# Performance work log

Hardware: AMD Instinct MI355X
Metric: run time of the kernel (lower is better)

Reference implementation:

```python
import jax, jax.numpy as jnp
import numpy as np

B, N, E = 2, 50000, 800000
IN_CH, SP_CH, OUT_CH, EDGE_CH = 64, 16, 32, 1


def _xavier(k, shape):
    scale = (2.0 / (shape[0] + shape[1])) ** 0.5
    return jax.random.normal(k, shape, dtype=jnp.float32) * scale


def setup_inputs() -> dict:
    key = jax.random.key(0)
    ks = jax.random.split(key, 20)
    return {
        "X": jax.random.normal(ks[0], (B, N, IN_CH), dtype=jnp.float32),
        "edge_index0": jax.random.randint(ks[1], (2, E), 0, N),
        "edge_index1": jax.random.randint(ks[2], (2, E), 0, N),
        "edge_weight0": jax.random.uniform(ks[3], (E, EDGE_CH), dtype=jnp.float32),
        "edge_weight1": jax.random.uniform(ks[4], (E, EDGE_CH), dtype=jnp.float32),
        "res_n_id0": jnp.arange(N),
        "res_n_id1": jnp.arange(N),
        # conv1 params (in=IN_CH, out=SP_CH)
        "value1": _xavier(ks[5], (IN_CH, SP_CH)),
        "key1": _xavier(ks[6], (SP_CH, SP_CH)),
        "query1": _xavier(ks[7], (SP_CH, SP_CH)),
        "we1": _xavier(ks[8], (EDGE_CH, SP_CH)),
        "att_w1": _xavier(ks[9], (3 * SP_CH, 1)),
        "att_b1": jnp.zeros((1,), jnp.float32),
        "cat_w1": _xavier(ks[10], (2 * SP_CH, SP_CH)),
        "cat_b1": jnp.zeros((SP_CH,), jnp.float32),
        # conv2 params (in=SP_CH, out=OUT_CH)
        "value2": _xavier(ks[11], (SP_CH, OUT_CH)),
        "key2": _xavier(ks[12], (OUT_CH, OUT_CH)),
        "query2": _xavier(ks[13], (OUT_CH, OUT_CH)),
        "we2": _xavier(ks[14], (EDGE_CH, OUT_CH)),
        "att_w2": _xavier(ks[15], (3 * OUT_CH, 1)),
        "att_b2": jnp.zeros((1,), jnp.float32),
        "cat_w2": _xavier(ks[16], (2 * OUT_CH, OUT_CH)),
        "cat_b2": jnp.zeros((OUT_CH,), jnp.float32),
    }


def _egnn_conv(Xs, Xd, ei, ef, value, key_w, query_w, we, att_w, att_b, cat_w, cat_b):
    # Xs: [B,Ns,Cin] source nodes, Xd: [B,Nd,Cin] dest nodes, ei: [2,E], ef: [E,edge_ch]
    xs = Xs @ value                       # [B,Ns,C]
    xd = Xd @ value                       # [B,Nd,C]
    e = ef @ we                           # [E,C]
    xj = xs[:, ei[0]]                     # [B,E,C] source gather
    xi = xd[:, ei[1]]                     # [B,E,C] dest gather
    q = xj @ query_w                      # note: original code names are swapped; kept faithful
    k = xi @ key_w
    att_in = jnp.concatenate([k, q, jnp.broadcast_to(e, q.shape)], axis=-1)  # [B,E,3C]
    att = jax.nn.sigmoid(att_in @ att_w + att_b)      # [B,E,1]
    msg = att * xj * jax.nn.sigmoid(e)                # [B,E,C]
    aggr = jnp.zeros(xd.shape, xd.dtype).at[:, ei[1]].add(msg)  # scatter-add over dest
    upd = jnp.concatenate([xd, aggr], axis=-1) @ cat_w + cat_b  # [B,Nd,C]
    return xd + jax.nn.relu(upd)


def reference(X, edge_index0, edge_index1, edge_weight0, edge_weight1,
              res_n_id0, res_n_id1,
              value1, key1, query1, we1, att_w1, att_b1, cat_w1, cat_b1,
              value2, key2, query2, we2, att_w2, att_b2, cat_w2, cat_b2):
    X1 = _egnn_conv(X, X[:, res_n_id0], edge_index0, edge_weight0,
                    value1, key1, query1, we1, att_w1, att_b1, cat_w1, cat_b1)
    X1 = jax.nn.leaky_relu(X1)  # negative_slope 0.01, matches torch default
    X2 = _egnn_conv(X1, X1[:, res_n_id1], edge_index1, edge_weight1,
                    value2, key2, query2, we2, att_w2, att_b2, cat_w2, cat_b2)
    return X2
```

## Files before the change

kernel.cpp:

```cpp
#include <hip/hip_runtime.h>
#include <hip/hip_fp16.h>

#define BB   2
#define NN   50000
#define EE   800000
#define INCH 64
#define C1   16
#define C2   32
#define NB   (BB*NN)

#define W1S   6
#define W2S   5
#define NBK1  ((NN + 63) >> 6)
#define NBK2  ((NN + 31) >> 5)
#define NBKT  (NBK1 + NBK2)
#define EB    4096
#define TPB   1024
#define NEBLK ((2*EE + EB - 1) / EB)

#define OFF_XS1   0
#define OFF_XS2   (OFF_XS1 + NB*C1/2)
#define OFF_DOTK1 (OFF_XS2 + NB*C2/2)
#define OFF_DOTQ1 (OFF_DOTK1 + NB)
#define OFF_DOTK2 (OFF_DOTQ1 + NB)
#define OFF_DOTQ2 (OFF_DOTK2 + NB)
#define OFF_AG1   (OFF_DOTQ2 + NB)
#define OFF_AG2   (OFF_AG1 + NN*32)
#define OFF_BTOT  (OFF_AG2 + NN*64)
#define OFF_BBASE (OFF_BTOT + NBKT)
#define OFF_START (OFF_BBASE + NBKT)
#define OFF_DEG   (OFF_START + 2*NN)
#define OFF_SC    (OFF_DEG + 2*NN)
#define OFF_RECS2 (OFF_SC + 2)
#define OFF_REGION (OFF_RECS2 + 2*EE*2)
#define OFF_RECS   OFF_REGION
#define OFF_BCNT   (OFF_REGION + 2*EE*2)
#define OFF_PREC   OFF_REGION

__device__ __forceinline__ float sigmoidf(float x) {
    return __builtin_amdgcn_rcpf(1.0f + __expf(-x));
}

__device__ __forceinline__ float h2f_u(unsigned u) {
    return __half2float(__ushort_as_half((unsigned short)u));
}

__global__ __launch_bounds__(TPB) void k_value1cnt(
        const float* __restrict__ X, const float* __restrict__ value1,
        const float* __restrict__ key1, const float* __restrict__ query1,
        const float* __restrict__ aw1,
        const int* __restrict__ ei0, const int* __restrict__ ei1,
        const float* __restrict__ we1, const float* __restrict__ we2,
        const float* __restrict__ aw2,
        __half* __restrict__ xs1h, float* __restrict__ dotk1,
        float* __restrict__ dotq1, unsigned* __restrict__ blockCnt,
        float* __restrict__ sc) {
    __shared__ float W[INCH*C1];
    __shared__ float KV[C1], QV[C1];
    __shared__ unsigned h[NBKT];
    int tid = threadIdx.x;
    if (tid < 256) {
        for (int i = tid; i < INCH*C1; i += 256) W[i] = value1[i];
        if (tid < C1) {
            float kv = 0.f, qv = 0.f;
#pragma unroll
            for (int j = 0; j < C1; ++j) {
                kv += key1[tid*C1+j]   * aw1[j];
                qv += query1[tid*C1+j] * aw1[C1+j];
            }
            KV[tid] = kv; QV[tid] = qv;
        }
    } else {
        for (int i = tid - 256; i < NBKT; i += 768) h[i] = 0u;
        if (blockIdx.x == 0 && tid == 256) {
            float e = 0.f;
            for (int j = 0; j < C1; ++j) e += we1[j] * aw1[2*C1+j];
            sc[0] = e;
        }
        if (blockIdx.x == 0 && tid == 257) {
            float e = 0.f;
            for (int j = 0; j < C2; ++j) e += we2[j] * aw2[2*C2+j];
            sc[1] = e;
        }
    }
    __syncthreads();
    if (tid < 256) {
        int bn = blockIdx.x * 256 + tid;
        if (bn < NB) {
            int b = (bn >= NN) ? 1 : 0;
            int node = bn - b*NN;
            const float4* Xr = (const float4*)(X + (size_t)bn * INCH);
            float acc[C1];
#pragma unroll
            for (int j = 0; j < C1; ++j) acc[j] = 0.f;
#pragma unroll
            for (int v = 0; v < 16; ++v) {
                float4 p = Xr[v];
                float x4[4] = {p.x, p.y, p.z, p.w};
#pragma unroll
                for (int hh = 0; hh < 4; ++hh) {
                    int i = v*4 + hh;
                    float xv = x4[hh];
#pragma unroll
                    for (int j = 0; j < C1; ++j) acc[j] += xv * W[i*C1+j];
                }
            }
            float dk = 0.f, dq = 0.f;
#pragma unroll
            for (int j = 0; j < C1; ++j) { dk += acc[j]*KV[j]; dq += acc[j]*QV[j]; }
            __half* o = xs1h + ((size_t)node * C1) * 2 + b;
#pragma unroll
            for (int j = 0; j < C1; ++j) o[2*j] = __float2half_rn(acc[j]);
            dotk1[node*2 + b] = dk; dotq1[node*2 + b] = dq;
        }
    } else {
        int base = blockIdx.x * EB;
        for (int j = tid - 256; j < EB; j += 768) {
            int t = base + j;
            if (t < 2*EE) {
                int bkt;
                if (t < EE) { int dst = ei0[EE + t];      bkt = dst >> W1S; }
                else        { int dst = ei1[EE + t - EE]; bkt = NBK1 + (dst >> W2S); }
                atomicAdd(&h[bkt], 1u);
            }
        }
    }
    __syncthreads();
    unsigned* o = blockCnt + (size_t)blockIdx.x * NBKT;
    for (int i = tid; i < NBKT; i += TPB) o[i] = h[i];
}

__global__ __launch_bounds__(512) void k_scanBkt(
        unsigned* __restrict__ blockCnt, unsigned* __restrict__ bktTot) {
    __shared__ unsigned s[512];
    int tid = threadIdx.x;
    int bkt = blockIdx.x;
    unsigned v = (tid < NEBLK) ? blockCnt[(size_t)tid * NBKT + bkt] : 0u;
    s[tid] = v;
    __syncthreads();
    for (int o = 1; o < 512; o <<= 1) {
        unsigned t = (tid >= o) ? s[tid - o] : 0u;
        __syncthreads();
        s[tid] += t;
        __syncthreads();
    }
    if (tid < NEBLK) blockCnt[(size_t)tid * NBKT + bkt] = s[tid] - v;
    if (tid == 511) bktTot[bkt] = s[511];
}

__global__ __launch_bounds__(1024) void k_scanTot(
        const unsigned* __restrict__ bktTot, unsigned* __restrict__ bucketBase) {
    __shared__ unsigned s[1024];
    int tid = threadIdx.x;
    int base = tid * 3;
    unsigned a0 = (base + 0 < NBKT) ? bktTot[base + 0] : 0u;
    unsigned a1 = (base + 1 < NBKT) ? bktTot[base + 1] : 0u;
    unsigned a2 = (base + 2 < NBKT) ? bktTot[base + 2] : 0u;
    unsigned l = a0 + a1 + a2;
    s[tid] = l;
    __syncthreads();
    for (int o = 1; o < 1024; o <<= 1) {
        unsigned t = (tid >= o) ? s[tid - o] : 0u;
        __syncthreads();
        s[tid] += t;
        __syncthreads();
    }
    unsigned ex = s[tid] - l;
    if (base + 0 < NBKT) bucketBase[base + 0] = ex;
    if (base + 1 < NBKT) bucketBase[base + 1] = ex + a0;
    if (base + 2 < NBKT) bucketBase[base + 2] = ex + a0 + a1;
}

__global__ __launch_bounds__(TPB) void k_permute(
        const int* __restrict__ ei0, const int* __restrict__ ei1,
        const float* __restrict__ ew0, const float* __restrict__ ew1,
        const unsigned* __restrict__ blockOff, const unsigned* __restrict__ bucketBase,
        uint2* __restrict__ recs) {
    __shared__ unsigned off[NBKT];
    __shared__ unsigned cur[NBKT];
    int tid = threadIdx.x;
    const unsigned* bo = blockOff + (size_t)blockIdx.x * NBKT;
    for (int i = tid; i < NBKT; i += TPB) { off[i] = bo[i] + bucketBase[i]; cur[i] = 0u; }
    __syncthreads();
    int base = blockIdx.x * EB;
#pragma unroll
    for (int j = 0; j < EB/TPB; ++j) {
        int t = base + j*TPB + tid;
        if (t >= 2*EE) break;
        int bkt, dl, src; float ef;
        if (t < EE) {
            int dst = ei0[EE + t];
            bkt = dst >> W1S; dl = dst & 63;
            src = ei0[t]; ef = ew0[t];
        } else {
            int e = t - EE;
            int dst = ei1[EE + e];
            bkt = NBK1 + (dst >> W2S); dl = dst & 31;
            src = ei1[e]; ef = ew1[e];
        }
        unsigned pos = off[bkt] + atomicAdd(&cur[bkt], 1u);
        recs[pos] = make_uint2((unsigned)src | ((unsigned)dl << 16), __float_as_uint(ef));
    }
}

__global__ __launch_bounds__(256) void k_sortbp(
        const uint2* __restrict__ recs, const unsigned* __restrict__ bktTot,
        const unsigned* __restrict__ bucketBase,
        const float* __restrict__ dotk1, const float* __restrict__ dotq1,
        const float* __restrict__ ab1, const float* __restrict__ sc,
        uint2* __restrict__ recs2, unsigned* __restrict__ startA,
        unsigned* __restrict__ degA) {
    __shared__ unsigned h[64], sOff[64], cur[64];
    int tid = threadIdx.x;
    int bkt = blockIdx.x;
    int lay1 = (bkt < NBK1) ? 1 : 0;
    int ndl  = lay1 ? 64 : 32;
    int nodeBase = lay1 ? (bkt << W1S) : ((bkt - NBK1) << W2S);
    int layOff   = lay1 ? 0 : NN;
    if (tid < 64) h[tid] = 0u;
    __syncthreads();
    unsigned cnt = bktTot[bkt], base = bucketBase[bkt];
    for (unsigned i = tid; i < cnt; i += 256)
        atomicAdd(&h[recs[base + i].x >> 16], 1u);
    __syncthreads();
    if (tid == 0) {
        unsigned run = 0;
        for (int d = 0; d < ndl; ++d) { sOff[d] = run; run += h[d]; }
    }
    __syncthreads();
    if (tid < ndl) {
        cur[tid] = sOff[tid];
        int node = nodeBase + tid;
        if (node < NN) {
            startA[layOff + node] = base + sOff[tid];
            degA[layOff + node]   = h[tid];
        }
    }
    __syncthreads();
    float ec = sc[0], ab0 = ab1[0];
    for (unsigned i = tid; i < cnt; i += 256) {
        uint2 r = recs[base + i];
        unsigned dl  = r.x >> 16;
        unsigned src = r.x & 0xffffu;
        unsigned pos = atomicAdd(&cur[dl], 1u);
        unsigned dst = (unsigned)nodeBase + dl;
        if (lay1) {
            float ef = __uint_as_float(r.y);
            float eb = ef * ec + ab0;
            float2 dk = *(const float2*)(dotk1 + dst*2);
            float2 dq = *(const float2*)(dotq1 + src*2);
            float p0 = sigmoidf(dk.x + dq.x + eb);
            float p1 = sigmoidf(dk.y + dq.y + eb);
            unsigned pu = __builtin_bit_cast(unsigned, __floats2half2_rn(p0, p1));
            unsigned eu = (unsigned)__half_as_ushort(__float2half_rn(ef));
            recs2[base + pos] = make_uint2(src | (pu << 16),
                                           (pu >> 16) | (eu << 16));
        } else {
            recs2[base + pos] = make_uint2(src | (dst << 16), r.y);
        }
    }
}

__global__ __launch_bounds__(256) void k_prep(
        const uint2* __restrict__ recs2seg, const float* __restrict__ dotk,
        const float* __restrict__ dotq, const float* __restrict__ ab,
        const float* __restrict__ sc, int scIdx, uint2* __restrict__ prec) {
    int e = blockIdx.x * 256 + threadIdx.x;
    uint2 r = recs2seg[e];
    int src = r.x & 0xffff, dst = r.x >> 16;
    float ef = __uint_as_float(r.y);
    float eb = ef * sc[scIdx] + ab[0];
    float2 dk = *(const float2*)(dotk + dst*2);
    float2 dq = *(const float2*)(dotq + src*2);
    float p0 = sigmoidf(dk.x + dq.x + eb);
    float p1 = sigmoidf(dk.y + dq.y + eb);
    unsigned pu = __builtin_bit_cast(unsigned, __floats2half2_rn(p0, p1));
    unsigned eu = (unsigned)__half_as_ushort(__float2half_rn(ef));
    prec[e] = make_uint2((unsigned)src | (pu << 16),
                         (pu >> 16) | (eu << 16));
}

__global__ __launch_bounds__(256) void k_aggr1f(
        const uint2* __restrict__ prec, const float* __restrict__ we,
        const uint2* __restrict__ xsh,
        const unsigned* __restrict__ startA, const unsigned* __restrict__ degA,
        float* __restrict__ aggrf) {
    int t = blockIdx.x * 256 + threadIdx.x;
    int node = t >> 4, sub = t & 15, cp = sub & 7, h = sub >> 3;
    unsigned s = startA[node];
    unsigned n = degA[node];
    float w0 = we[2*cp], w1 = we[2*cp+1];
    float a0 = 0.f, a1 = 0.f, a2 = 0.f, a3 = 0.f;
    unsigned i = (unsigned)h;
    uint2 r_n = make_uint2(0u, 0u); uint2 xr_n = make_uint2(0u, 0u);
    if (i < n) {
        r_n  = prec[s + i];
        xr_n = xsh[(size_t)(r_n.x & 0xffff)*8 + cp];
    }
    for (; i < n; i += 2) {
        uint2 r = r_n; uint2 xr = xr_n;
        if (i + 2 < n) {
            r_n  = prec[s + i + 2];
            xr_n = xsh[(size_t)(r_n.x & 0xffff)*8 + cp];
        }
        float p0 = h2f_u(r.x >> 16);
        float p1 = h2f_u(r.y & 0xffff);
        float ef = h2f_u(r.y >> 16);
        float se0 = sigmoidf(ef * w0);
        float se1 = sigmoidf(ef * w1);
        float2 f0 = __half22float2(__builtin_bit_cast(__half2, xr.x));
        float2 f1 = __half22float2(__builtin_bit_cast(__half2, xr.y));
        a0 += p0 * se0 * f0.x;
        a1 += p1 * se0 * f0.y;
        a2 += p0 * se1 * f1.x;
        a3 += p1 * se1 * f1.y;
    }
    a0 += __shfl_xor(a0, 8); a1 += __shfl_xor(a1, 8);
    a2 += __shfl_xor(a2, 8); a3 += __shfl_xor(a3, 8);
    if (h == 0)
        ((float4*)aggrf)[(size_t)node*8 + cp] = make_float4(a0, a1, a2, a3);
}

__global__ __launch_bounds__(256) void k_update1(
        const float* __restrict__ cat_w, const float* __restrict__ cat_b,
        const float* __restrict__ value2,
        const float* __restrict__ key2, const float* __restrict__ query2,
        const float* __restrict__ aw2,
        const __half* __restrict__ xs1h, const float* __restrict__ aggr1f,
        __half* __restrict__ xs2h, float* __restrict__ dotk2, float* __restrict__ dotq2) {
    __shared__ float CW[2*C1*C1];
    __shared__ float CB[C1];
    __shared__ float V2[C1*C2];
    __shared__ float KV[C2], QV[C2];
    int tid = threadIdx.x;
    for (int i = tid; i < 2*C1*C1; i += 256) CW[i] = cat_w[i];
    for (int i = tid; i < C1*C2;   i += 256) V2[i] = value2[i];
    if (tid < C1) CB[tid] = cat_b[tid];
    if (tid < C2) {
        float kv = 0.f;
#pragma unroll
        for (int j = 0; j < C2; ++j) kv += key2[tid*C2+j] * aw2[j];
        KV[tid] = kv;
    } else if (tid < 2*C2) {
        int c = tid - C2;
        float qv = 0.f;
#pragma unroll
        for (int j = 0; j < C2; ++j) qv += query2[c*C2+j] * aw2[C2+j];
        QV[c] = qv;
    }
    __syncthreads();
    int bn = blockIdx.x * 256 + tid;
    if (bn >= NB) return;
    int b = (bn >= NN) ? 1 : 0;
    int node = bn - b*NN;
    int bs = b * 16;
    float xd[C1], ag[C1];
    {
        const uint4* xv = (const uint4*)(xs1h + (size_t)node * C1 * 2);
#pragma unroll
        for (int v = 0; v < 4; ++v) {
            uint4 q = xv[v];
            xd[4*v+0] = h2f_u(q.x >> bs);
            xd[4*v+1] = h2f_u(q.y >> bs);
            xd[4*v+2] = h2f_u(q.z >> bs);
            xd[4*v+3] = h2f_u(q.w >> bs);
        }
    }
    {
        const float4* av = (const float4*)(aggr1f + (size_t)node * 32);
#pragma unroll
        for (int w = 0; w < 8; ++w) {
            float4 f = av[w];
            ag[2*w]   = b ? f.y : f.x;
            ag[2*w+1] = b ? f.w : f.z;
        }
    }
    float x1[C1];
#pragma unroll
    for (int j = 0; j < C1; ++j) {
        float u = CB[j];
#pragma unroll
        for (int i = 0; i < C1; ++i) {
            u += xd[i] * CW[i*C1 + j];
            u += ag[i] * CW[(C1+i)*C1 + j];
        }
        float o = xd[j] + fmaxf(u, 0.f);
        x1[j] = (o > 0.f) ? o : 0.01f * o;
    }
    float o2[C2];
#pragma unroll
    for (int k = 0; k < C2; ++k) o2[k] = 0.f;
#pragma unroll
    for (int j = 0; j < C1; ++j) {
        float xv = x1[j];
#pragma unroll
        for (int k = 0; k < C2; ++k) o2[k] += xv * V2[j*C2 + k];
    }
    float dk = 0.f, dq = 0.f;
#pragma unroll
    for (int k = 0; k < C2; ++k) { dk += o2[k]*KV[k]; dq += o2[k]*QV[k]; }
    __half* o = xs2h + ((size_t)node*C2)*2 + b;
#pragma unroll
    for (int k = 0; k < C2; ++k) o[2*k] = __float2half_rn(o2[k]);
    dotk2[node*2 + b] = dk; dotq2[node*2 + b] = dq;
}

__global__ __launch_bounds__(256) void k_aggr2f(
        const uint2* __restrict__ prec, const float* __restrict__ we,
        const uint2* __restrict__ xsh,
        const unsigned* __restrict__ startA, const unsigned* __restrict__ degA,
        float* __restrict__ aggrf) {
    int t = blockIdx.x * 256 + threadIdx.x;
    int node = t >> 5, sub = t & 31, cp = sub & 15, h = sub >> 4;
    unsigned s = startA[NN + node] - EE;
    unsigned n = degA[NN + node];
    float w0 = we[2*cp], w1 = we[2*cp+1];
    float a0 = 0.f, a1 = 0.f, a2 = 0.f, a3 = 0.f;
    unsigned i = (unsigned)h;
    uint2 r_n = make_uint2(0u, 0u); uint2 xr_n = make_uint2(0u, 0u);
    if (i < n) {
        r_n  = prec[s + i];
        xr_n = xsh[(size_t)(r_n.x & 0xffff)*16 + cp];
    }
    for (; i < n; i += 2) {
        uint2 r = r_n; uint2 xr = xr_n;
        if (i + 2 < n) {
            r_n  = prec[s + i + 2];
            xr_n = xsh[(size_t)(r_n.x & 0xffff)*16 + cp];
        }
        float p0 = h2f_u(r.x >> 16);
        float p1 = h2f_u(r.y & 0xffff);
        float ef = h2f_u(r.y >> 16);
        float se0 = sigmoidf(ef * w0);
        float se1 = sigmoidf(ef * w1);
        float2 f0 = __half22float2(__builtin_bit_cast(__half2, xr.x));
        float2 f1 = __half22float2(__builtin_bit_cast(__half2, xr.y));
        a0 += p0 * se0 * f0.x;
        a1 += p1 * se0 * f0.y;
        a2 += p0 * se1 * f1.x;
        a3 += p1 * se1 * f1.y;
    }
    a0 += __shfl_xor(a0, 16); a1 += __shfl_xor(a1, 16);
    a2 += __shfl_xor(a2, 16); a3 += __shfl_xor(a3, 16);
    if (h == 0)
        ((float4*)aggrf)[(size_t)node*16 + cp] = make_float4(a0, a1, a2, a3);
}

__global__ __launch_bounds__(256) void k_update2(
        const float* __restrict__ cat_w, const float* __restrict__ cat_b,
        const __half* __restrict__ xs2h, const float* __restrict__ aggr2f,
        float* __restrict__ out) {
    __shared__ float CW[2*C2*C2];
    __shared__ float CB[C2];
    int tid = threadIdx.x;
    for (int i = tid; i < 2*C2*C2; i += 256) CW[i] = cat_w[i];
    if (tid < C2) CB[tid] = cat_b[tid];
    __syncthreads();
    int bn = blockIdx.x * 256 + tid;
    if (bn >= NB) return;
    int b = (bn >= NN) ? 1 : 0;
    int node = bn - b*NN;
    int bs = b * 16;
    float xd[C2], ag[C2];
    {
        const uint4* xv = (const uint4*)(xs2h + (size_t)node * C2 * 2);
#pragma unroll
        for (int v = 0; v < 8; ++v) {
            uint4 q = xv[v];
            xd[4*v+0] = h2f_u(q.x >> bs);
            xd[4*v+1] = h2f_u(q.y >> bs);
            xd[4*v+2] = h2f_u(q.z >> bs);
            xd[4*v+3] = h2f_u(q.w >> bs);
        }
    }
    {
        const float4* av = (const float4*)(aggr2f + (size_t)node * 64);
#pragma unroll
        for (int w = 0; w < 16; ++w) {
            float4 f = av[w];
            ag[2*w]   = b ? f.y : f.x;
            ag[2*w+1] = b ? f.w : f.z;
        }
    }
    float o[C2];
#pragma unroll
    for (int k = 0; k < C2; ++k) {
        float u = CB[k];
#pragma unroll
        for (int i = 0; i < C2; ++i) {
            u += xd[i] * CW[i*C2 + k];
            u += ag[i] * CW[(C2+i)*C2 + k];
        }
        o[k] = xd[k] + fmaxf(u, 0.f);
    }
    float4* dst = (float4*)(out + (size_t)bn * C2);
#pragma unroll
    for (int v = 0; v < 8; ++v)
        dst[v] = make_float4(o[4*v], o[4*v+1], o[4*v+2], o[4*v+3]);
}

extern "C" void kernel_launch(void* const* d_in, const int* in_sizes, int n_in,
                              void* d_out, int out_size, void* d_ws, size_t ws_size,
                              hipStream_t stream) {
    const float* X      = (const float*)d_in[0];
    const int*   ei0    = (const int*)d_in[1];
    const int*   ei1    = (const int*)d_in[2];
    const float* ew0    = (const float*)d_in[3];
    const float* ew1    = (const float*)d_in[4];
    const float* value1 = (const float*)d_in[7];
    const float* key1   = (const float*)d_in[8];
    const float* query1 = (const float*)d_in[9];
    const float* we1    = (const float*)d_in[10];
    const float* aw1    = (const float*)d_in[11];
    const float* ab1    = (const float*)d_in[12];
    const float* cw1    = (const float*)d_in[13];
    const float* cb1    = (const float*)d_in[14];
    const float* value2 = (const float*)d_in[15];
    const float* key2   = (const float*)d_in[16];
    const float* query2 = (const float*)d_in[17];
    const float* we2    = (const float*)d_in[18];
    const float* aw2    = (const float*)d_in[19];
    const float* ab2    = (const float*)d_in[20];
    const float* cw2    = (const float*)d_in[21];
    const float* cb2    = (const float*)d_in[22];
    float* ws  = (float*)d_ws;
    float* out = (float*)d_out;

    __half* xs1h = (__half*)(ws + OFF_XS1);
    __half* xs2h = (__half*)(ws + OFF_XS2);
    float* aggr1f = ws + OFF_AG1;
    float* aggr2f = ws + OFF_AG2;
    unsigned* blockCnt   = (unsigned*)(ws + OFF_BCNT);
    unsigned* bktTot     = (unsigned*)(ws + OFF_BTOT);
    unsigned* bucketBase = (unsigned*)(ws + OFF_BBASE);
    unsigned* startA     = (unsigned*)(ws + OFF_START);
    unsigned* degA       = (unsigned*)(ws + OFF_DEG);
    uint2*    recs2      = (uint2*)(ws + OFF_RECS2);
    uint2*    recs       = (uint2*)(ws + OFF_RECS);
    uint2*    prec2      = (uint2*)(ws + OFF_PREC);

    k_value1cnt<<<NEBLK, TPB, 0, stream>>>(X, value1, key1, query1, aw1,
                                           ei0, ei1, we1, we2, aw2,
                                           xs1h, ws + OFF_DOTK1, ws + OFF_DOTQ1,
                                           blockCnt, ws + OFF_SC);

    k_scanBkt<<<NBKT, 512, 0, stream>>>(blockCnt, bktTot);
    k_scanTot<<<1, 1024, 0, stream>>>(bktTot, bucketBase);
    k_permute<<<NEBLK, TPB, 0, stream>>>(ei0, ei1, ew0, ew1,
                                         blockCnt, bucketBase, recs);
    k_sortbp<<<NBKT, 256, 0, stream>>>(recs, bktTot, bucketBase,
                                       ws + OFF_DOTK1, ws + OFF_DOTQ1,
                                       ab1, ws + OFF_SC,
                                       recs2, startA, degA);

    k_aggr1f<<<(NN*16)/256, 256, 0, stream>>>(recs2, we1, (const uint2*)xs1h,
                                              startA, degA, aggr1f);
    k_update1<<<(NB+255)/256, 256, 0, stream>>>(cw1, cb1, value2, key2, query2, aw2,
                                                xs1h, aggr1f,
                                                xs2h, ws + OFF_DOTK2, ws + OFF_DOTQ2);

    k_prep<<<EE/256, 256, 0, stream>>>(recs2 + EE, ws + OFF_DOTK2, ws + OFF_DOTQ2,
                                       ab2, ws + OFF_SC, 1, prec2);
    k_aggr2f<<<(NN*32)/256, 256, 0, stream>>>(prec2, we2, (const uint2*)xs2h,
                                              startA, degA, aggr2f);
    k_update2<<<(NB+255)/256, 256, 0, stream>>>(cw2, cb2, xs2h, aggr2f, out);
}
```

Baseline: 308.9 us.

## Fuse layer-2 aggregation with update via shared-memory staging

Result: faster. 292.9 us (-5.2%).

```diff
diff --git a/kernel.cpp b/kernel.cpp
--- a/kernel.cpp
+++ b/kernel.cpp
@@ -405,13 +405,22 @@
     dotk2[node*2 + b] = dk; dotq2[node*2 + b] = dq;
 }
 
-__global__ __launch_bounds__(256) void k_aggr2f(
+__global__ __launch_bounds__(256) void k_aggr2u(
         const uint2* __restrict__ prec, const float* __restrict__ we,
         const uint2* __restrict__ xsh,
         const unsigned* __restrict__ startA, const unsigned* __restrict__ degA,
-        float* __restrict__ aggrf) {
-    int t = blockIdx.x * 256 + threadIdx.x;
-    int node = t >> 5, sub = t & 31, cp = sub & 15, h = sub >> 4;
+        const float* __restrict__ cat_w, const float* __restrict__ cat_b,
+        const __half* __restrict__ xs2h, float* __restrict__ out) {
+    __shared__ float CW[2*C2*C2];
+    __shared__ float CB[C2];
+    __shared__ float agS[8*64];
+    __shared__ float xdS[8*2*32];
+    int tid = threadIdx.x;
+    for (int i = tid; i < 2*C2*C2; i += 256) CW[i] = cat_w[i];
+    if (tid < C2) CB[tid] = cat_b[tid];
+
+    int nl = tid >> 5, sub = tid & 31, cp = sub & 15, h = sub >> 4;
+    int node = blockIdx.x * 8 + nl;
     unsigned s = startA[NN + node] - EE;
     unsigned n = degA[NN + node];
     float w0 = we[2*cp], w1 = we[2*cp+1];
@@ -443,60 +452,33 @@
     a0 += __shfl_xor(a0, 16); a1 += __shfl_xor(a1, 16);
     a2 += __shfl_xor(a2, 16); a3 += __shfl_xor(a3, 16);
     if (h == 0)
-        ((float4*)aggrf)[(size_t)node*16 + cp] = make_float4(a0, a1, a2, a3);
-}
-
-__global__ __launch_bounds__(256) void k_update2(
-        const float* __restrict__ cat_w, const float* __restrict__ cat_b,
-        const __half* __restrict__ xs2h, const float* __restrict__ aggr2f,
-        float* __restrict__ out) {
-    __shared__ float CW[2*C2*C2];
-    __shared__ float CB[C2];
-    int tid = threadIdx.x;
-    for (int i = tid; i < 2*C2*C2; i += 256) CW[i] = cat_w[i];
-    if (tid < C2) CB[tid] = cat_b[tid];
-    __syncthreads();
-    int bn = blockIdx.x * 256 + tid;
-    if (bn >= NB) return;
-    int b = (bn >= NN) ? 1 : 0;
-    int node = bn - b*NN;
-    int bs = b * 16;
-    float xd[C2], ag[C2];
+        ((float4*)agS)[nl*16 + cp] = make_float4(a0, a1, a2, a3);
+
     {
-        const uint4* xv = (const uint4*)(xs2h + (size_t)node * C2 * 2);
-#pragma unroll
-        for (int v = 0; v < 8; ++v) {
-            uint4 q = xv[v];
-            xd[4*v+0] = h2f_u(q.x >> bs);
-            xd[4*v+1] = h2f_u(q.y >> bs);
-            xd[4*v+2] = h2f_u(q.z >> bs);
-            xd[4*v+3] = h2f_u(q.w >> bs);
-        }
-    }
-    {
-        const float4* av = (const float4*)(aggr2f + (size_t)node * 64);
-#pragma unroll
-        for (int w = 0; w < 16; ++w) {
-            float4 f = av[w];
-            ag[2*w]   = b ? f.y : f.x;
-            ag[2*w+1] = b ? f.w : f.z;
-        }
-    }
-    float o[C2];
-#pragma unroll
-    for (int k = 0; k < C2; ++k) {
-        float u = CB[k];
-#pragma unroll
-        for (int i = 0; i < C2; ++i) {
-            u += xd[i] * CW[i*C2 + k];
-            u += ag[i] * CW[(C2+i)*C2 + k];
-        }
-        o[k] = xd[k] + fmaxf(u, 0.f);
-    }
-    float4* dst = (float4*)(out + (size_t)bn * C2);
-#pragma unroll
-    for (int v = 0; v < 8; ++v)
-        dst[v] = make_float4(o[4*v], o[4*v+1], o[4*v+2], o[4*v+3]);
+        unsigned w = ((const unsigned*)(xs2h))[(size_t)(blockIdx.x*8) * 32 + tid];
+        int snl = tid >> 5, sc_ = tid & 31;
+        xdS[(snl*2 + 0)*32 + sc_] = h2f_u(w);
+        xdS[(snl*2 + 1)*32 + sc_] = h2f_u(w >> 16);
+    }
+    __syncthreads();
+
+    int b  = (tid >> 4) & 1;
+    int kk = tid & 15;
+    const float* xdp = &xdS[(nl*2 + b)*32];
+    const float* agp = &agS[nl*64];
+    float u0 = CB[kk], u1 = CB[kk+16];
+#pragma unroll
+    for (int ii = 0; ii < C2; ++ii) {
+        float xv = xdp[ii];
+        float av = agp[(ii>>1)*4 + (ii&1)*2 + b];
+        u0 += xv * CW[ii*C2 + kk]        + av * CW[(C2+ii)*C2 + kk];
+        u1 += xv * CW[ii*C2 + kk + 16]   + av * CW[(C2+ii)*C2 + kk + 16];
+    }
+    float o0 = xdp[kk]    + fmaxf(u0, 0.f);
+    float o1 = xdp[kk+16] + fmaxf(u1, 0.f);
+    float* orow = out + ((size_t)(b*NN + node)) * C2;
+    orow[kk]      = o0;
+    orow[kk + 16] = o1;
 }
 
 extern "C" void kernel_launch(void* const* d_in, const int* in_sizes, int n_in,
@@ -529,7 +511,6 @@
     __half* xs1h = (__half*)(ws + OFF_XS1);
     __half* xs2h = (__half*)(ws + OFF_XS2);
     float* aggr1f = ws + OFF_AG1;
-    float* aggr2f = ws + OFF_AG2;
     unsigned* blockCnt   = (unsigned*)(ws + OFF_BCNT);
     unsigned* bktTot     = (unsigned*)(ws + OFF_BTOT);
     unsigned* bucketBase = (unsigned*)(ws + OFF_BBASE);
@@ -561,7 +542,6 @@
 
     k_prep<<<EE/256, 256, 0, stream>>>(recs2 + EE, ws + OFF_DOTK2, ws + OFF_DOTQ2,
                                        ab2, ws + OFF_SC, 1, prec2);
-    k_aggr2f<<<(NN*32)/256, 256, 0, stream>>>(prec2, we2, (const uint2*)xs2h,
-                                              startA, degA, aggr2f);
-    k_update2<<<(NB+255)/256, 256, 0, stream>>>(cw2, cb2, xs2h, aggr2f, out);
-}
+    k_aggr2u<<<NN/8, 256, 0, stream>>>(prec2, we2, (const uint2*)xs2h,
+                                       startA, degA, cw2, cb2, xs2h, out);
+}
```
